# Performance work log

Measured on AMD Instinct MI355X. Metric: run time of the kernel, lower is better.

The kernel has to match this reference:

```python
import jax, jax.numpy as jnp
import numpy as np

B, S, H, KV, D = 1, 2048, 16, 4, 128
HID = H * D
CACHE = 2048
EPS = 1e-6
SCALE = 128 ** -0.5  # query_pre_attn_scalar ** -0.5
NEG = -1e9


def setup_inputs() -> dict:
    key = jax.random.key(0)
    ks = jax.random.split(key, 12)
    hidden_states = jax.random.normal(ks[0], (B, S, HID), jnp.float32)
    # rotary embeddings (Gemma3 style, base 10000, half-dim frequencies)
    pos = jnp.arange(S, dtype=jnp.float32)[:, None]
    inv_freq = 1.0 / (10000.0 ** (jnp.arange(0, D, 2, dtype=jnp.float32) / D))
    freqs = pos * inv_freq[None, :]
    emb = jnp.concatenate([freqs, freqs], axis=-1)  # [S, D]
    cos = jnp.cos(emb)[None]  # [1, S, D]
    sin = jnp.sin(emb)[None]
    # additive causal mask [B, 1, S, S]
    r = jnp.arange(S)
    attention_mask = jnp.where(r[:, None] >= r[None, :], 0.0, NEG).astype(jnp.float32)[None, None]
    lyra_key_cache = jax.random.normal(ks[1], (1, KV, CACHE, D), jnp.float32)
    lyra_value_cache = jax.random.normal(ks[2], (1, KV, CACHE, D), jnp.float32)
    w = 0.02
    Wq = jax.random.normal(ks[3], (H * D, HID), jnp.float32) * w
    Wk = jax.random.normal(ks[4], (KV * D, HID), jnp.float32) * w
    Wv = jax.random.normal(ks[5], (KV * D, HID), jnp.float32) * w
    Wo = jax.random.normal(ks[6], (HID, H * D), jnp.float32) * w
    q_norm_w = jax.random.normal(ks[7], (D,), jnp.float32) * 0.1
    k_norm_w = jax.random.normal(ks[8], (D,), jnp.float32) * 0.1
    return dict(hidden_states=hidden_states, cos=cos, sin=sin,
                attention_mask=attention_mask,
                lyra_key_cache=lyra_key_cache, lyra_value_cache=lyra_value_cache,
                Wq=Wq, Wk=Wk, Wv=Wv, Wo=Wo, q_norm_w=q_norm_w, k_norm_w=k_norm_w)


def _rmsnorm(x, w):
    xf = x.astype(jnp.float32)
    n = xf * jax.lax.rsqrt(jnp.mean(xf * xf, axis=-1, keepdims=True) + EPS)
    return (n * (1.0 + w.astype(jnp.float32))).astype(x.dtype)


def _rotate_half(x):
    h = x.shape[-1] // 2
    return jnp.concatenate([-x[..., h:], x[..., :h]], axis=-1)


def _rope(x, c, s):
    return x * c + _rotate_half(x) * s


def _attend(q, k, v, mask, n_rep):
    # q: [B,h,Sq,D]; k,v: [B,KV,Sk,D]; mask additive float broadcastable to [B,h,Sq,Sk]
    k = jnp.repeat(k, n_rep, axis=1)
    v = jnp.repeat(v, n_rep, axis=1)
    w = jnp.einsum('bhqd,bhkd->bhqk', q, k) * SCALE + mask
    w = jax.nn.softmax(w.astype(jnp.float32), axis=-1).astype(q.dtype)
    out = jnp.einsum('bhqk,bhkd->bhqd', w, v)
    return out, w


def reference(hidden_states, cos, sin, attention_mask, lyra_key_cache,
              lyra_value_cache, Wq, Wk, Wv, Wo, q_norm_w, k_norm_w):
    bsz, q_len, _ = hidden_states.shape
    q = (hidden_states @ Wq.T).reshape(bsz, q_len, H, D).transpose(0, 2, 1, 3)
    k = (hidden_states @ Wk.T).reshape(bsz, q_len, KV, D).transpose(0, 2, 1, 3)
    v = (hidden_states @ Wv.T).reshape(bsz, q_len, KV, D).transpose(0, 2, 1, 3)
    q = _rmsnorm(q, q_norm_w)
    k = _rmsnorm(k, k_norm_w)
    vanilla_q, lyra_q = q[:, :H // 2], q[:, H // 2:]
    c = cos[:, None]  # [B,1,S,D]
    s = sin[:, None]
    n_rep = (H // 2) // KV  # stream_num_key_value_groups
    # vanilla stream
    vanilla_q_rope = _rope(vanilla_q, c, s)
    k_rope = _rope(k, c, s)
    vanilla_out, vanilla_w = _attend(vanilla_q_rope, k_rope, v, attention_mask, n_rep)
    # lyra stream: prepend static KV cache; bool mask added as float (faithful to source)
    lyra_q_rope = _rope(lyra_q, c, s)
    lk = jnp.concatenate([jnp.broadcast_to(lyra_key_cache, (bsz, KV, CACHE, D)), k_rope], axis=2)
    lv = jnp.concatenate([jnp.broadcast_to(lyra_value_cache, (bsz, KV, CACHE, D)), v], axis=2)
    rows = jnp.arange(q_len)[:, None]
    cols = jnp.arange(CACHE + q_len)[None, :]
    lyra_mask = (rows < cols - CACHE).astype(jnp.float32)[None, None]  # True -> +1.0, as in torch code
    lyra_out, _ = _attend(lyra_q_rope, lk, lv, lyra_mask, n_rep)
    combined = jnp.concatenate([vanilla_out, lyra_out], axis=1)  # [B,H,S,D]
    combined = combined.transpose(0, 2, 1, 3).reshape(bsz, q_len, H * D)
    attn_output = combined @ Wo.T
    return attn_output, vanilla_w
```

## Files before the change

kernel.cpp:

```cpp
#include <hip/hip_runtime.h>
#include <math.h>

#define S_LEN 2048
#define HID 2048
#define NH 16
#define NKV 4
#define DH 128
#define CACHE_LEN 2048
#define QKV_W 3072
#define SCALE 0.08838834764831845f
#define EPS 1e-6f
#define LYRA_C 12.0f

typedef short bf16x8 __attribute__((ext_vector_type(8)));
typedef float f32x4 __attribute__((ext_vector_type(4)));

static __device__ __forceinline__ short f2bf(float x) {
  union { float f; unsigned u; } v; v.f = x;
  unsigned r = (v.u + 0x7FFF + ((v.u >> 16) & 1)) >> 16;
  return (short)r;
}

static __device__ __forceinline__ float bf2f(short h) {
  union { unsigned u; float f; } v;
  v.u = ((unsigned)(unsigned short)h) << 16;
  return v.f;
}

#define GLDS16(g, l)                                                      \
  __builtin_amdgcn_global_load_lds(                                       \
      (const __attribute__((address_space(1))) unsigned int*)(g),         \
      (__attribute__((address_space(3))) unsigned int*)(l), 16, 0, 0)

__global__ __launch_bounds__(256) void pack_bf16(
    const float* __restrict__ src, short* __restrict__ dst) {
  const int i = (blockIdx.x * 256 + threadIdx.x) * 8;
  float4 a = *(const float4*)(src + i);
  float4 b = *(const float4*)(src + i + 4);
  bf16x8 o;
  o[0] = f2bf(a.x); o[1] = f2bf(a.y); o[2] = f2bf(a.z); o[3] = f2bf(a.w);
  o[4] = f2bf(b.x); o[5] = f2bf(b.y); o[6] = f2bf(b.z); o[7] = f2bf(b.w);
  *(bf16x8*)(dst + i) = o;
}

__global__ __launch_bounds__(256) void gemm_bf16(
    const short* __restrict__ A, const short* __restrict__ B,
    float* __restrict__ C, int K, int ldc) {
  __shared__ short sA[4096];
  __shared__ short sB[4096];
  const int t = threadIdx.x;
  const int w = t >> 6;
  const int lane = t & 63;
  const int quad = lane >> 4;
  const int l16 = lane & 15;
  const int tm = blockIdx.y * 128;
  const int tn = blockIdx.x * 128;
  const int srow = lane >> 2;
  const int scol = (lane & 3) * 8;
  const int mblk = (w & 1) * 64;
  const int nblk = (w >> 1) * 64;
  f32x4 acc[4][4];
#pragma unroll
  for (int i = 0; i < 4; ++i)
#pragma unroll
    for (int j = 0; j < 4; ++j) acc[i][j] = (f32x4){0.f, 0.f, 0.f, 0.f};

  const short* Ab = A + (size_t)(tm + w * 32 + srow) * K + scol;
  const short* Bb = B + (size_t)(tn + w * 32 + srow) * K + scol;
  const size_t rstep = (size_t)16 * K;

  for (int k0 = 0; k0 < K; k0 += 32) {
    GLDS16(Ab + k0, sA + (w * 2 + 0) * 512);
    GLDS16(Ab + rstep + k0, sA + (w * 2 + 1) * 512);
    GLDS16(Bb + k0, sB + (w * 2 + 0) * 512);
    GLDS16(Bb + rstep + k0, sB + (w * 2 + 1) * 512);
    __syncthreads();
    bf16x8 af[4], bfv[4];
#pragma unroll
  for (int ms = 0; ms < 4; ++ms)
      af[ms] = *(const bf16x8*)&sA[(mblk + ms * 16 + l16) * 32 + quad * 8];
#pragma unroll
    for (int ns = 0; ns < 4; ++ns)
      bfv[ns] = *(const bf16x8*)&sB[(nblk + ns * 16 + l16) * 32 + quad * 8];
#pragma unroll
    for (int ms = 0; ms < 4; ++ms)
#pragma unroll
      for (int ns = 0; ns < 4; ++ns)
        acc[ms][ns] = __builtin_amdgcn_mfma_f32_16x16x32_bf16(
            af[ms], bfv[ns], acc[ms][ns], 0, 0, 0);
    __syncthreads();
  }
#pragma unroll
  for (int ms = 0; ms < 4; ++ms)
#pragma unroll
    for (int ns = 0; ns < 4; ++ns) {
      const int row = tm + mblk + ms * 16 + quad * 4;
      const int col = tn + nblk + ns * 16 + l16;
#pragma unroll
      for (int r = 0; r < 4; ++r)
        C[(size_t)(row + r) * ldc + col] = acc[ms][ns][r];
    }
}

__global__ __launch_bounds__(256) void rms_rope(
    float* __restrict__ qkv,
    const float* __restrict__ cosb, const float* __restrict__ sinb,
    const float* __restrict__ qw, const float* __restrict__ kw) {
  const int unit = blockIdx.x * 4 + (threadIdx.x >> 6);
  const int lane = threadIdx.x & 63;
  const int total_q = S_LEN * NH;
  float* base;
  const float* w;
  int pos;
  if (unit < total_q) {
    pos = unit >> 4;
    int head = unit & 15;
    base = qkv + (size_t)pos * QKV_W + head * DH;
    w = qw;
  } else {
    int u = unit - total_q;
    pos = u >> 2;
    int head = u & 3;
    base = qkv + (size_t)pos * QKV_W + 2048 + head * DH;
    w = kw;
  }
  float x0 = base[lane];
  float x1 = base[lane + 64];
  float ss = x0 * x0 + x1 * x1;
#pragma unroll
  for (int off = 32; off > 0; off >>= 1) ss += __shfl_xor(ss, off);
  float r = rsqrtf(ss * (1.0f / 128.0f) + EPS);
  float n0 = x0 * r * (1.0f + w[lane]);
  float n1 = x1 * r * (1.0f + w[lane + 64]);
  float c0 = cosb[(size_t)pos * DH + lane];
  float c1 = cosb[(size_t)pos * DH + lane + 64];
  float s0 = sinb[(size_t)pos * DH + lane];
  float s1 = sinb[(size_t)pos * DH + lane + 64];
  base[lane]      = n0 * c0 - n1 * s0;
  base[lane + 64] = n1 * c1 + n0 * s1;
}

__global__ __launch_bounds__(256) void pack_k(
    const float* __restrict__ qkv, const float* __restrict__ kcache,
    short* __restrict__ Kbf, short* __restrict__ Klo) {
  const int idx = blockIdx.x * 256 + threadIdx.x;
  const int e4 = idx * 4;
  const int kvh = e4 >> 19;
  const int rem = e4 & ((1 << 19) - 1);
  const int key = rem >> 7;
  const int d = rem & 127;
  const int dsw = d ^ ((key & 7) << 3);
  if (key < CACHE_LEN) {
    float4 v = *(const float4*)(kcache + (((size_t)kvh * CACHE_LEN + key) << 7) + d);
    short4 o;
    o.x = f2bf(v.x); o.y = f2bf(v.y); o.z = f2bf(v.z); o.w = f2bf(v.w);
    *(short4*)(Kbf + (size_t)(e4 - d) + dsw) = o;
  } else {
    float4 v = *(const float4*)(qkv + (size_t)(key - CACHE_LEN) * QKV_W + 2048 + kvh * DH + d);
    short4 o;
    o.x = f2bf(v.x); o.y = f2bf(v.y); o.z = f2bf(v.z); o.w = f2bf(v.w);
    *(short4*)(Kbf + (size_t)(e4 - d) + dsw) = o;
    short4 ol;
    ol.x = f2bf(v.x - bf2f(o.x));
    ol.y = f2bf(v.y - bf2f(o.y));
    ol.z = f2bf(v.z - bf2f(o.z));
    ol.w = f2bf(v.w - bf2f(o.w));
    *(short4*)(Klo + ((size_t)kvh * 2048 + (key - CACHE_LEN)) * 128 + dsw) = ol;
  }
}

__global__ __launch_bounds__(256) void pack_vt(
    const float* __restrict__ qkv, const float* __restrict__ vcache,
    short* __restrict__ Vt) {
  __shared__ float tile[64][65];
  const int key0 = blockIdx.x * 64;
  const int d0 = blockIdx.y * 64;
  const int kvh = blockIdx.z;
  const int t = threadIdx.x;
  const int c = t & 63;
  const int r0 = t >> 6;
#pragma unroll
  for (int i = 0; i < 16; ++i) {
    int r = r0 + i * 4;
    int key = key0 + r;
    float v;
    if (key < CACHE_LEN)
      v = vcache[(((size_t)kvh * CACHE_LEN + key) << 7) + d0 + c];
    else
      v = qkv[(size_t)(key - CACHE_LEN) * QKV_W + 2560 + kvh * DH + d0 + c];
    tile[r][c] = v;
  }
  __syncthreads();
#pragma unroll
  for (int i = 0; i < 16; ++i) {
    int wr = r0 + i * 4;
    int csw = c ^ (((d0 + wr) & 7) << 3);
    Vt[((size_t)kvh * DH + d0 + wr) * 4096 + key0 + csw] = f2bf(tile[c][wr]);
  }
}

static __device__ __forceinline__ void stage_kv128(
    const short* Kb, const short* Vb, short* buf, int key0, int w, int lane) {
#pragma unroll
  for (int i = 0; i < 4; ++i)
    GLDS16(Kb + ((size_t)key0 + w * 16 + i * 4) * 128 + lane * 8,
           buf + (w * 16 + i * 4) * 128);
#pragma unroll
  for (int i = 0; i < 4; ++i)
    GLDS16(Vb + (size_t)(w * 16 + i * 4 + (lane >> 4)) * 4096 + key0 +
               (lane & 15) * 8,
           buf + 16384 + (w * 16 + i * 4) * 128);
}

__global__ __launch_bounds__(512) void lyra_attn(
    const float* __restrict__ qkv,
    const short* __restrict__ Kbf,
    const short* __restrict__ Vtb,
    short* __restrict__ combined_bf) {
  __shared__ short sKV[2][32768];
  __shared__ short sP[8][2][1024];
  const int hj = blockIdx.x;
  const int qt = blockIdx.y;
  const int kvh = hj >> 1;
  const int t = threadIdx.x;
  const int w = t >> 6;
  const int lane = t & 63;
  const int quad = lane >> 4;
  const int l16 = lane & 15;
  const int wr = w >> 2;
  const int wc = w & 3;
  const int row0 = qt * 64;
  const int swx = (l16 & 7) << 4;
  const int voff = (wc >> 1) * 128 + ((((wc & 1) * 64) + quad * 16) ^ swx);

  bf16x8 qf[2][4];
#pragma unroll
  for (int g = 0; g < 2; ++g) {
    const float* qrow =
        qkv + (size_t)(row0 + wr * 32 + g * 16 + l16) * QKV_W + (8 + hj) * DH;
#pragma unroll
    for (int ks = 0; ks < 4; ++ks) {
      float4 f0 = *(const float4*)(qrow + ks * 32 + quad * 8);
      float4 f1 = *(const float4*)(qrow + ks * 32 + quad * 8 + 4);
      qf[g][ks][0] = f2bf(f0.x * SCALE); qf[g][ks][1] = f2bf(f0.y * SCALE);
      qf[g][ks][2] = f2bf(f0.z * SCALE); qf[g][ks][3] = f2bf(f0.w * SCALE);
      qf[g][ks][4] = f2bf(f1.x * SCALE); qf[g][ks][5] = f2bf(f1.y * SCALE);
      qf[g][ks][6] = f2bf(f1.z * SCALE); qf[g][ks][7] = f2bf(f1.w * SCALE);
    }
  }
  bf16x8 onesf;
#pragma unroll
  for (int i = 0; i < 8; ++i) onesf[i] = (short)0x3F80;

  f32x4 accO[2][8];
#pragma unroll
  for (int g = 0; g < 2; ++g)
#pragma unroll
    for (int i = 0; i < 8; ++i) accO[g][i] = (f32x4){0.f, 0.f, 0.f, 0.f};
  f32x4 accL[2];
  accL[0] = (f32x4){0.f, 0.f, 0.f, 0.f};
  accL[1] = (f32x4){0.f, 0.f, 0.f, 0.f};

  const short* Kb = Kbf + (size_t)kvh * 4096 * DH;
  const short* Vb = Vtb + (size_t)kvh * DH * 4096;

  stage_kv128(Kb, Vb, &sKV[0][0], 0, w, lane);

  int b = 0;
  for (int kt = 0; kt < 32; ++kt) {
    asm volatile("s_waitcnt vmcnt(0)" ::: "memory");
    __builtin_amdgcn_s_barrier();
    __builtin_amdgcn_sched_barrier(0);

    if (kt < 31)
      stage_kv128(Kb, Vb, &sKV[b ^ 1][0], (kt + 1) * 128, w, lane);

    const char* Ksc = (const char*)&sKV[b][0];
    const char* Vsc = (const char*)&sKV[b][16384];

    f32x4 accS[2][2];
#pragma unroll
    for (int g = 0; g < 2; ++g)
#pragma unroll
      for (int s = 0; s < 2; ++s)
        accS[g][s] = (f32x4){-LYRA_C, -LYRA_C, -LYRA_C, -LYRA_C};
    __builtin_amdgcn_s_setprio(1);
#pragma unroll
    for (int s = 0; s < 2; ++s) {
      const char* krow = Ksc + (wc * 32 + s * 16 + l16) * 256;
#pragma unroll
      for (int ks = 0; ks < 4; ++ks) {
        bf16x8 bk = *(const bf16x8*)(krow + ((ks * 64 + quad * 16) ^ swx));
        accS[0][s] = __builtin_amdgcn_mfma_f32_16x16x32_bf16(qf[0][ks], bk, accS[0][s], 0, 0, 0);
        accS[1][s] = __builtin_amdgcn_mfma_f32_16x16x32_bf16(qf[1][ks], bk, accS[1][s], 0, 0, 0);
      }
    }
    __builtin_amdgcn_s_setprio(0);

    const int base = kt * 128 + wc * 32;
#pragma unroll
    for (int g = 0; g < 2; ++g) {
      short* sPg = &sP[w][g][0];
#pragma unroll
      for (int s = 0; s < 2; ++s) {
        const int col = base + s * 16 + l16;
#pragma unroll
        for (int r = 0; r < 4; ++r) {
          const int row = quad * 4 + r;
          const int grow = row0 + wr * 32 + g * 16 + row;
          float z = accS[g][s][r];
          if ((col - CACHE_LEN) > grow) z += 1.0f;
          const int sl = (s * 2 + (l16 >> 3)) ^ (row & 7);
          sPg[row * 64 + sl * 8 + (l16 & 7)] = f2bf(__expf(z));
        }
      }
    }

    __builtin_amdgcn_s_setprio(1);
    bf16x8 ap0 = *(const bf16x8*)&sP[w][0][l16 * 64 + ((quad ^ (l16 & 7)) << 3)];
    bf16x8 ap1 = *(const bf16x8*)&sP[w][1][l16 * 64 + ((quad ^ (l16 & 7)) << 3)];
    accL[0] = __builtin_amdgcn_mfma_f32_16x16x32_bf16(ap0, onesf, accL[0], 0, 0, 0);
    accL[1] = __builtin_amdgcn_mfma_f32_16x16x32_bf16(ap1, onesf, accL[1], 0, 0, 0);
#pragma unroll
    for (int t8 = 0; t8 < 8; ++t8) {
      bf16x8 bv = *(const bf16x8*)(Vsc + (t8 * 16 + l16) * 256 + voff);
      accO[0][t8] = __builtin_amdgcn_mfma_f32_16x16x32_bf16(ap0, bv, accO[0][t8], 0, 0, 0);
      accO[1][t8] = __builtin_amdgcn_mfma_f32_16x16x32_bf16(ap1, bv, accO[1][t8], 0, 0, 0);
    }
    __builtin_amdgcn_s_setprio(0);

    b ^= 1;
  }

  __syncthreads();
  float* sO = (float*)&sKV[0][0];
  float* sLa = (float*)&sP[0][0][0];
  if (wc != 0) {
    float* dst = sO + (size_t)(wc - 1) * 8192;
#pragma unroll
    for (int g = 0; g < 2; ++g)
#pragma unroll
      for (int t8 = 0; t8 < 8; ++t8)
#pragma unroll
        for (int r = 0; r < 4; ++r) {
          const int rl = wr * 32 + g * 16 + quad * 4 + r;
          dst[rl * 128 + t8 * 16 + l16] = accO[g][t8][r];
        }
    if (l16 == 0) {
#pragma unroll
      for (int g = 0; g < 2; ++g)
#pragma unroll
        for (int r = 0; r < 4; ++r)
          sLa[(wc - 1) * 64 + wr * 32 + g * 16 + quad * 4 + r] = accL[g][r];
    }
  }
  __syncthreads();
  if (wc == 0) {
#pragma unroll
    for (int g = 0; g < 2; ++g) {
      float linv[4];
#pragma unroll
      for (int r = 0; r < 4; ++r) {
        const int rl = wr * 32 + g * 16 + quad * 4 + r;
        linv[r] = 1.0f / (accL[g][r] + sLa[rl] + sLa[64 + rl] + sLa[128 + rl]);
      }
#pragma unroll
      for (int t8 = 0; t8 < 8; ++t8)
#pragma unroll
        for (int r = 0; r < 4; ++r) {
          const int rl = wr * 32 + g * 16 + quad * 4 + r;
          const int c = t8 * 16 + l16;
          float o = accO[g][t8][r] + sO[rl * 128 + c] + sO[8192 + rl * 128 + c] +
                    sO[16384 + rl * 128 + c];
          combined_bf[(size_t)(row0 + rl) * HID + (8 + hj) * DH + c] =
              f2bf(o * linv[r]);
        }
    }
  }
}

__global__ __launch_bounds__(512) void vanilla_attn(
    const float* __restrict__ qkv,
    const short* __restrict__ Kbf,
    const short* __restrict__ Klo,
    const short* __restrict__ Vtb,
    float* __restrict__ wout,
    float* __restrict__ vinv,
    short* __restrict__ combined_bf) {
  __shared__ short sKV[2][32768];
  __shared__ short sP[8][2][1024];
  const int hj = blockIdx.x;
  const int qt = blockIdx.y;
  const int kvh = hj >> 1;
  const int t = threadIdx.x;
  const int w = t >> 6;
  const int lane = t & 63;
  const int quad = lane >> 4;
  const int l16 = lane & 15;
  const int wr = w >> 2;
  const int wc = w & 3;
  const int row0 = qt * 64;
  const int swx = (l16 & 7) << 4;
  const int voff = (wc >> 1) * 128 + ((((wc & 1) * 64) + quad * 16) ^ swx);
  const int nt = qt / 2 + 1;

  bf16x8 qh[2][4], ql[2][4];
#pragma unroll
  for (int g = 0; g < 2; ++g) {
    const float* qrow =
        qkv + (size_t)(row0 + wr * 32 + g * 16 + l16) * QKV_W + hj * DH;
#pragma unroll
    for (int ks = 0; ks < 4; ++ks) {
#pragma unroll
      for (int e = 0; e < 8; ++e) {
        float x = qrow[ks * 32 + quad * 8 + e] * SCALE;
        short h = f2bf(x);
        qh[g][ks][e] = h;
        ql[g][ks][e] = f2bf(x - bf2f(h));
      }
    }
  }

  f32x4 accO[2][8];
#pragma unroll
  for (int g = 0; g < 2; ++g)
#pragma unroll
    for (int i = 0; i < 8; ++i) accO[g][i] = (f32x4){0.f, 0.f, 0.f, 0.f};
  float accR[2][4] = {{0.f, 0.f, 0.f, 0.f}, {0.f, 0.f, 0.f, 0.f}};

  const short* Kh = Kbf + ((size_t)kvh * 4096 + 2048) * DH;
  const short* Kl = Klo + (size_t)kvh * 2048 * DH;
  const short* Vb = Vtb + (size_t)kvh * DH * 4096 + 2048;
  float* wrow = wout + (size_t)hj * S_LEN * S_LEN;

  stage_kv128(Kh, Vb, &sKV[0][0], 0, w, lane);

  int b = 0;
  for (int kt = 0; kt < nt; ++kt) {
    asm volatile("s_waitcnt vmcnt(0)" ::: "memory");
    __builtin_amdgcn_s_barrier();
    __builtin_amdgcn_sched_barrier(0);

    if (kt < nt - 1)
      stage_kv128(Kh, Vb, &sKV[b ^ 1][0], (kt + 1) * 128, w, lane);

    const int key0 = kt * 128;
    bf16x8 klf[2][4];
#pragma unroll
    for (int s = 0; s < 2; ++s)
#pragma unroll
      for (int ks = 0; ks < 4; ++ks)
        klf[s][ks] = *(const bf16x8*)(
            Kl + (size_t)(key0 + wc * 32 + s * 16 + l16) * 128 +
            ((ks * 32 + quad * 8) ^ ((l16 & 7) << 3)));

    const char* Khs = (const char*)&sKV[b][0];
    const char* Vsc = (const char*)&sKV[b][16384];

    f32x4 accS[2][2];
#pragma unroll
    for (int g = 0; g < 2; ++g)
#pragma unroll
      for (int s = 0; s < 2; ++s)
        accS[g][s] = (f32x4){-LYRA_C, -LYRA_C, -LYRA_C, -LYRA_C};
    __builtin_amdgcn_s_setprio(1);
#pragma unroll
    for (int s = 0; s < 2; ++s) {
      const char* krh = Khs + (wc * 32 + s * 16 + l16) * 256;
#pragma unroll
      for (int ks = 0; ks < 4; ++ks) {
        bf16x8 kh = *(const bf16x8*)(krh + ((ks * 64 + quad * 16) ^ swx));
        accS[0][s] = __builtin_amdgcn_mfma_f32_16x16x32_bf16(qh[0][ks], kh, accS[0][s], 0, 0, 0);
        accS[1][s] = __builtin_amdgcn_mfma_f32_16x16x32_bf16(qh[1][ks], kh, accS[1][s], 0, 0, 0);
        accS[0][s] = __builtin_amdgcn_mfma_f32_16x16x32_bf16(ql[0][ks], kh, accS[0][s], 0, 0, 0);
        accS[1][s] = __builtin_amdgcn_mfma_f32_16x16x32_bf16(ql[1][ks], kh, accS[1][s], 0, 0, 0);
        accS[0][s] = __builtin_amdgcn_mfma_f32_16x16x32_bf16(qh[0][ks], klf[s][ks], accS[0][s], 0, 0, 0);
        accS[1][s] = __builtin_amdgcn_mfma_f32_16x16x32_bf16(qh[1][ks], klf[s][ks], accS[1][s], 0, 0, 0);
      }
    }
    __builtin_amdgcn_s_setprio(0);

    const bool diag = (kt == nt - 1);
#pragma unroll
    for (int g = 0; g < 2; ++g) {
      short* sPg = &sP[w][g][0];
      float pr[4] = {0.f, 0.f, 0.f, 0.f};
#pragma unroll
      for (int s = 0; s < 2; ++s) {
        const int col = key0 + wc * 32 + s * 16 + l16;
#pragma unroll
        for (int r = 0; r < 4; ++r) {
          const int row = quad * 4 + r;
          const int grow = row0 + wr * 32 + g * 16 + row;
          float p = __expf(accS[g][s][r]);
          if (diag && col > grow) p = 0.f;
          pr[r] += p;
          const int sl = (s * 2 + (l16 >> 3)) ^ (row & 7);
          sPg[row * 64 + sl * 8 + (l16 & 7)] = f2bf(p);
          wrow[(size_t)grow * S_LEN + col] = p;
        }
      }
#pragma unroll
      for (int r = 0; r < 4; ++r) {
        float v = pr[r];
        v += __shfl_xor(v, 1);
        v += __shfl_xor(v, 2);
        v += __shfl_xor(v, 4);
        v += __shfl_xor(v, 8);
        accR[g][r] += v;
      }
    }

    __builtin_amdgcn_s_setprio(1);
    bf16x8 ap0 = *(const bf16x8*)&sP[w][0][l16 * 64 + ((quad ^ (l16 & 7)) << 3)];
    bf16x8 ap1 = *(const bf16x8*)&sP[w][1][l16 * 64 + ((quad ^ (l16 & 7)) << 3)];
#pragma unroll
    for (int t8 = 0; t8 < 8; ++t8) {
      bf16x8 bv = *(const bf16x8*)(Vsc + (t8 * 16 + l16) * 256 + voff);
      accO[0][t8] = __builtin_amdgcn_mfma_f32_16x16x32_bf16(ap0, bv, accO[0][t8], 0, 0, 0);
      accO[1][t8] = __builtin_amdgcn_mfma_f32_16x16x32_bf16(ap1, bv, accO[1][t8], 0, 0, 0);
    }
    __builtin_amdgcn_s_setprio(0);

    b ^= 1;
  }

  __syncthreads();
  float* sO = (float*)&sKV[0][0];
  float* sLa = (float*)&sP[0][0][0];
  if (wc != 0) {
    float* dst = sO + (size_t)(wc - 1) * 8192;
#pragma unroll
    for (int g = 0; g < 2; ++g)
#pragma unroll
      for (int t8 = 0; t8 < 8; ++t8)
#pragma unroll
        for (int r = 0; r < 4; ++r) {
          const int rl = wr * 32 + g * 16 + quad * 4 + r;
          dst[rl * 128 + t8 * 16 + l16] = accO[g][t8][r];
        }
    if (l16 == 0) {
#pragma unroll
      for (int g = 0; g < 2; ++g)
#pragma unroll
        for (int r = 0; r < 4; ++r)
          sLa[(wc - 1) * 64 + wr * 32 + g * 16 + quad * 4 + r] = accR[g][r];
    }
  }
  __syncthreads();
  if (wc == 0) {
#pragma unroll
    for (int g = 0; g < 2; ++g) {
      float linv[4];
#pragma unroll
      for (int r = 0; r < 4; ++r) {
        const int rl = wr * 32 + g * 16 + quad * 4 + r;
        linv[r] = 1.0f / (accR[g][r] + sLa[rl] + sLa[64 + rl] + sLa[128 + rl]);
      }
      if (l16 == 0) {
#pragma unroll
        for (int r = 0; r < 4; ++r)
          vinv[hj * S_LEN + row0 + wr * 32 + g * 16 + quad * 4 + r] = linv[r];
      }
#pragma unroll
      for (int t8 = 0; t8 < 8; ++t8)
#pragma unroll
        for (int r = 0; r < 4; ++r) {
          const int rl = wr * 32 + g * 16 + quad * 4 + r;
          const int c = t8 * 16 + l16;
          float o = accO[g][t8][r] + sO[rl * 128 + c] + sO[8192 + rl * 128 + c] +
                    sO[16384 + rl * 128 + c];
          combined_bf[(size_t)(row0 + rl) * HID + hj * DH + c] =
              f2bf(o * linv[r]);
        }
    }
  }
}

__global__ __launch_bounds__(256) void vnorm(
    const float* __restrict__ vinv, float* __restrict__ wout) {
  const int row = blockIdx.x;
  const int h = blockIdx.y;
  float* p = wout + (size_t)h * S_LEN * S_LEN + (size_t)row * S_LEN;
  const float inv = vinv[h * S_LEN + row];
  const int t = threadIdx.x;
#pragma unroll
  for (int i = 0; i < 2; ++i) {
    const int j = (t + i * 256) * 4;
    float4 v;
    if (j > row) {
      v = make_float4(0.f, 0.f, 0.f, 0.f);
    } else if (j + 3 <= row) {
      v = *(const float4*)(p + j);
      v.x *= inv; v.y *= inv; v.z *= inv; v.w *= inv;
    } else {
      v = *(const float4*)(p + j);
      v.x = (j + 0 <= row) ? v.x * inv : 0.f;
      v.y = (j + 1 <= row) ? v.y * inv : 0.f;
      v.z = (j + 2 <= row) ? v.z * inv : 0.f;
      v.w = (j + 3 <= row) ? v.w * inv : 0.f;
    }
    *(float4*)(p + j) = v;
  }
}

extern "C" void kernel_launch(void* const* d_in, const int* in_sizes, int n_in,
                              void* d_out, int out_size, void* d_ws, size_t ws_size,
                              hipStream_t stream) {
  (void)in_sizes; (void)n_in; (void)out_size; (void)ws_size;
  const float* hidden = (const float*)d_in[0];
  const float* cosb   = (const float*)d_in[1];
  const float* sinb   = (const float*)d_in[2];
  const float* kcache = (const float*)d_in[4];
  const float* vcache = (const float*)d_in[5];
  const float* Wq = (const float*)d_in[6];
  const float* Wk = (const float*)d_in[7];
  const float* Wv = (const float*)d_in[8];
  const float* Wo = (const float*)d_in[9];
  const float* qw = (const float*)d_in[10];
  const float* kw = (const float*)d_in[11];

  float* out  = (float*)d_out;
  float* wout = out + (size_t)4194304;

  float* qkv = (float*)d_ws;
  short* Kbf = (short*)(qkv + (size_t)2048 * QKV_W);
  short* Vtb = Kbf + (size_t)4 * 4096 * DH;
  short* combined_bf = Vtb + (size_t)4 * DH * 4096;
  short* Wo_bf = combined_bf + (size_t)2048 * HID;

  short* hidden_bf = (short*)wout;
  short* Wqkv_bf = hidden_bf + (size_t)2048 * HID;

  short* Klo  = (short*)out;
  float* vinv = (float*)(Klo + (size_t)4 * 2048 * DH);

  pack_bf16<<<dim3(2048), 256, 0, stream>>>(hidden, hidden_bf);
  pack_bf16<<<dim3(2048), 256, 0, stream>>>(Wq, Wqkv_bf);
  pack_bf16<<<dim3(512), 256, 0, stream>>>(Wk, Wqkv_bf + (size_t)2048 * 2048);
  pack_bf16<<<dim3(512), 256, 0, stream>>>(Wv, Wqkv_bf + (size_t)2560 * 2048);
  pack_bf16<<<dim3(2048), 256, 0, stream>>>(Wo, Wo_bf);

  gemm_bf16<<<dim3(24, 16), 256, 0, stream>>>(hidden_bf, Wqkv_bf, qkv, 2048, QKV_W);
  rms_rope<<<dim3(10240), 256, 0, stream>>>(qkv, cosb, sinb, qw, kw);
  pack_k<<<dim3(2048), 256, 0, stream>>>(qkv, kcache, Kbf, Klo);
  pack_vt<<<dim3(64, 2, 4), 256, 0, stream>>>(qkv, vcache, Vtb);
  lyra_attn<<<dim3(8, 32), 512, 0, stream>>>(qkv, Kbf, Vtb, combined_bf);
  vanilla_attn<<<dim3(8, 32), 512, 0, stream>>>(qkv, Kbf, Klo, Vtb, wout, vinv,
                                                combined_bf);
  vnorm<<<dim3(2048, 8), 256, 0, stream>>>(vinv, wout);
  gemm_bf16<<<dim3(16, 16), 256, 0, stream>>>(combined_bf, Wo_bf, out, 2048, HID);
}
```

Measured before the change: 495.9 us.

## Merge pack, attention and output-GEMM/vnorm launches into fewer fused kernels

Combines the five bf16 pack launches into one kernel, merges K and V packing into one launch, and runs lyra and vanilla attention as one grid with the stream chosen by block index. The output projection GEMM and the attention-weight normalisation are also merged into one launch. This cuts launch gaps and lets independent work run concurrently, but uniform-branch kernels now carry the LDS and register footprint of their largest branch. Klo and vinv move from the output buffer into workspace so the merged GEMM can write the output while vnorm reads vinv.

```diff
diff --git a/kernel.cpp b/kernel.cpp
--- a/kernel.cpp
+++ b/kernel.cpp
@@ -32,14 +32,26 @@
       (const __attribute__((address_space(1))) unsigned int*)(g),         \
       (__attribute__((address_space(3))) unsigned int*)(l), 16, 0, 0)
 
-__global__ __launch_bounds__(256) void pack_bf16(
-    const float* __restrict__ src, short* __restrict__ dst) {
-  const int i = (blockIdx.x * 256 + threadIdx.x) * 8;
+__global__ __launch_bounds__(256) void pack_all(
+    const float* __restrict__ hidden, const float* __restrict__ Wq,
+    const float* __restrict__ Wk, const float* __restrict__ Wv,
+    const float* __restrict__ Wo, short* __restrict__ hidden_bf,
+    short* __restrict__ Wqkv_bf, short* __restrict__ Wo_bf) {
+  const int b = blockIdx.x;
+  const float* src;
+  short* dst;
+  int off;
+  if (b < 2048)      { src = hidden; dst = hidden_bf; off = b; }
+  else if (b < 4096) { src = Wq; dst = Wqkv_bf; off = b - 2048; }
+  else if (b < 4608) { src = Wk; dst = Wqkv_bf + (size_t)2048 * 2048; off = b - 4096; }
+  else if (b < 5120) { src = Wv; dst = Wqkv_bf + (size_t)2560 * 2048; off = b - 4608; }
+  else               { src = Wo; dst = Wo_bf; off = b - 5120; }
+  const int i = (off * 256 + threadIdx.x) * 8;
   float4 a = *(const float4*)(src + i);
-  float4 b = *(const float4*)(src + i + 4);
+  float4 c = *(const float4*)(src + i + 4);
   bf16x8 o;
   o[0] = f2bf(a.x); o[1] = f2bf(a.y); o[2] = f2bf(a.z); o[3] = f2bf(a.w);
-  o[4] = f2bf(b.x); o[5] = f2bf(b.y); o[6] = f2bf(b.z); o[7] = f2bf(b.w);
+  o[4] = f2bf(c.x); o[5] = f2bf(c.y); o[6] = f2bf(c.z); o[7] = f2bf(c.w);
   *(bf16x8*)(dst + i) = o;
 }
 
@@ -77,7 +89,7 @@
     __syncthreads();
     bf16x8 af[4], bfv[4];
 #pragma unroll
-  for (int ms = 0; ms < 4; ++ms)
+    for (int ms = 0; ms < 4; ++ms)
       af[ms] = *(const bf16x8*)&sA[(mblk + ms * 16 + l16) * 32 + quad * 8];
 #pragma unroll
     for (int ns = 0; ns < 4; ++ns)
@@ -140,62 +152,63 @@
   base[lane + 64] = n1 * c1 + n0 * s1;
 }
 
-__global__ __launch_bounds__(256) void pack_k(
+__global__ __launch_bounds__(256) void pack_kv(
     const float* __restrict__ qkv, const float* __restrict__ kcache,
-    short* __restrict__ Kbf, short* __restrict__ Klo) {
-  const int idx = blockIdx.x * 256 + threadIdx.x;
-  const int e4 = idx * 4;
-  const int kvh = e4 >> 19;
-  const int rem = e4 & ((1 << 19) - 1);
-  const int key = rem >> 7;
-  const int d = rem & 127;
-  const int dsw = d ^ ((key & 7) << 3);
-  if (key < CACHE_LEN) {
-    float4 v = *(const float4*)(kcache + (((size_t)kvh * CACHE_LEN + key) << 7) + d);
-    short4 o;
-    o.x = f2bf(v.x); o.y = f2bf(v.y); o.z = f2bf(v.z); o.w = f2bf(v.w);
-    *(short4*)(Kbf + (size_t)(e4 - d) + dsw) = o;
+    const float* __restrict__ vcache, short* __restrict__ Kbf,
+    short* __restrict__ Klo, short* __restrict__ Vt) {
+  __shared__ float tile[64][65];
+  const int b = blockIdx.x;
+  const int t = threadIdx.x;
+  if (b < 2048) {
+    const int idx = b * 256 + t;
+    const int e4 = idx * 4;
+    const int kvh = e4 >> 19;
+    const int rem = e4 & ((1 << 19) - 1);
+    const int key = rem >> 7;
+    const int d = rem & 127;
+    const int dsw = d ^ ((key & 7) << 3);
+    if (key < CACHE_LEN) {
+      float4 v = *(const float4*)(kcache + (((size_t)kvh * CACHE_LEN + key) << 7) + d);
+      short4 o;
+      o.x = f2bf(v.x); o.y = f2bf(v.y); o.z = f2bf(v.z); o.w = f2bf(v.w);
+      *(short4*)(Kbf + (size_t)(e4 - d) + dsw) = o;
+    } else {
+      float4 v = *(const float4*)(qkv + (size_t)(key - CACHE_LEN) * QKV_W + 2048 + kvh * DH + d);
+      short4 o;
+      o.x = f2bf(v.x); o.y = f2bf(v.y); o.z = f2bf(v.z); o.w = f2bf(v.w);
+      *(short4*)(Kbf + (size_t)(e4 - d) + dsw) = o;
+      short4 ol;
+      ol.x = f2bf(v.x - bf2f(o.x));
+      ol.y = f2bf(v.y - bf2f(o.y));
+      ol.z = f2bf(v.z - bf2f(o.z));
+      ol.w = f2bf(v.w - bf2f(o.w));
+      *(short4*)(Klo + ((size_t)kvh * 2048 + (key - CACHE_LEN)) * 128 + dsw) = ol;
+    }
   } else {
-    float4 v = *(const float4*)(qkv + (size_t)(key - CACHE_LEN) * QKV_W + 2048 + kvh * DH + d);
-    short4 o;
-    o.x = f2bf(v.x); o.y = f2bf(v.y); o.z = f2bf(v.z); o.w = f2bf(v.w);
-    *(short4*)(Kbf + (size_t)(e4 - d) + dsw) = o;
-    short4 ol;
-    ol.x = f2bf(v.x - bf2f(o.x));
-    ol.y = f2bf(v.y - bf2f(o.y));
-    ol.z = f2bf(v.z - bf2f(o.z));
-    ol.w = f2bf(v.w - bf2f(o.w));
-    *(short4*)(Klo + ((size_t)kvh * 2048 + (key - CACHE_LEN)) * 128 + dsw) = ol;
-  }
-}
-
-__global__ __launch_bounds__(256) void pack_vt(
-    const float* __restrict__ qkv, const float* __restrict__ vcache,
-    short* __restrict__ Vt) {
-  __shared__ float tile[64][65];
-  const int key0 = blockIdx.x * 64;
-  const int d0 = blockIdx.y * 64;
-  const int kvh = blockIdx.z;
-  const int t = threadIdx.x;
-  const int c = t & 63;
-  const int r0 = t >> 6;
-#pragma unroll
-  for (int i = 0; i < 16; ++i) {
-    int r = r0 + i * 4;
-    int key = key0 + r;
-    float v;
-    if (key < CACHE_LEN)
-      v = vcache[(((size_t)kvh * CACHE_LEN + key) << 7) + d0 + c];
-    else
-      v = qkv[(size_t)(key - CACHE_LEN) * QKV_W + 2560 + kvh * DH + d0 + c];
-    tile[r][c] = v;
-  }
-  __syncthreads();
-#pragma unroll
-  for (int i = 0; i < 16; ++i) {
-    int wr = r0 + i * 4;
-    int csw = c ^ (((d0 + wr) & 7) << 3);
-    Vt[((size_t)kvh * DH + d0 + wr) * 4096 + key0 + csw] = f2bf(tile[c][wr]);
+    const int j = b - 2048;
+    const int key0 = (j & 63) * 64;
+    const int d0 = ((j >> 6) & 1) * 64;
+    const int kvh = j >> 7;
+    const int c = t & 63;
+    const int r0 = t >> 6;
+#pragma unroll
+    for (int i = 0; i < 16; ++i) {
+      int r = r0 + i * 4;
+      int key = key0 + r;
+      float v;
+      if (key < CACHE_LEN)
+        v = vcache[(((size_t)kvh * CACHE_LEN + key) << 7) + d0 + c];
+      else
+        v = qkv[(size_t)(key - CACHE_LEN) * QKV_W + 2560 + kvh * DH + d0 + c];
+      tile[r][c] = v;
+    }
+    __syncthreads();
+#pragma unroll
+    for (int i = 0; i < 16; ++i) {
+      int wr = r0 + i * 4;
+      int csw = c ^ (((d0 + wr) & 7) << 3);
+      Vt[((size_t)kvh * DH + d0 + wr) * 4096 + key0 + csw] = f2bf(tile[c][wr]);
+    }
   }
 }
 
@@ -212,174 +225,7 @@
            buf + 16384 + (w * 16 + i * 4) * 128);
 }
 
-__global__ __launch_bounds__(512) void lyra_attn(
-    const float* __restrict__ qkv,
-    const short* __restrict__ Kbf,
-    const short* __restrict__ Vtb,
-    short* __restrict__ combined_bf) {
-  __shared__ short sKV[2][32768];
-  __shared__ short sP[8][2][1024];
-  const int hj = blockIdx.x;
-  const int qt = blockIdx.y;
-  const int kvh = hj >> 1;
-  const int t = threadIdx.x;
-  const int w = t >> 6;
-  const int lane = t & 63;
-  const int quad = lane >> 4;
-  const int l16 = lane & 15;
-  const int wr = w >> 2;
-  const int wc = w & 3;
-  const int row0 = qt * 64;
-  const int swx = (l16 & 7) << 4;
-  const int voff = (wc >> 1) * 128 + ((((wc & 1) * 64) + quad * 16) ^ swx);
-
-  bf16x8 qf[2][4];
-#pragma unroll
-  for (int g = 0; g < 2; ++g) {
-    const float* qrow =
-        qkv + (size_t)(row0 + wr * 32 + g * 16 + l16) * QKV_W + (8 + hj) * DH;
-#pragma unroll
-    for (int ks = 0; ks < 4; ++ks) {
-      float4 f0 = *(const float4*)(qrow + ks * 32 + quad * 8);
-      float4 f1 = *(const float4*)(qrow + ks * 32 + quad * 8 + 4);
-      qf[g][ks][0] = f2bf(f0.x * SCALE); qf[g][ks][1] = f2bf(f0.y * SCALE);
-      qf[g][ks][2] = f2bf(f0.z * SCALE); qf[g][ks][3] = f2bf(f0.w * SCALE);
-      qf[g][ks][4] = f2bf(f1.x * SCALE); qf[g][ks][5] = f2bf(f1.y * SCALE);
-      qf[g][ks][6] = f2bf(f1.z * SCALE); qf[g][ks][7] = f2bf(f1.w * SCALE);
-    }
-  }
-  bf16x8 onesf;
-#pragma unroll
-  for (int i = 0; i < 8; ++i) onesf[i] = (short)0x3F80;
-
-  f32x4 accO[2][8];
-#pragma unroll
-  for (int g = 0; g < 2; ++g)
-#pragma unroll
-    for (int i = 0; i < 8; ++i) accO[g][i] = (f32x4){0.f, 0.f, 0.f, 0.f};
-  f32x4 accL[2];
-  accL[0] = (f32x4){0.f, 0.f, 0.f, 0.f};
-  accL[1] = (f32x4){0.f, 0.f, 0.f, 0.f};
-
-  const short* Kb = Kbf + (size_t)kvh * 4096 * DH;
-  const short* Vb = Vtb + (size_t)kvh * DH * 4096;
-
-  stage_kv128(Kb, Vb, &sKV[0][0], 0, w, lane);
-
-  int b = 0;
-  for (int kt = 0; kt < 32; ++kt) {
-    asm volatile("s_waitcnt vmcnt(0)" ::: "memory");
-    __builtin_amdgcn_s_barrier();
-    __builtin_amdgcn_sched_barrier(0);
-
-    if (kt < 31)
-      stage_kv128(Kb, Vb, &sKV[b ^ 1][0], (kt + 1) * 128, w, lane);
-
-    const char* Ksc = (const char*)&sKV[b][0];
-    const char* Vsc = (const char*)&sKV[b][16384];
-
-    f32x4 accS[2][2];
-#pragma unroll
-    for (int g = 0; g < 2; ++g)
-#pragma unroll
-      for (int s = 0; s < 2; ++s)
-        accS[g][s] = (f32x4){-LYRA_C, -LYRA_C, -LYRA_C, -LYRA_C};
-    __builtin_amdgcn_s_setprio(1);
-#pragma unroll
-    for (int s = 0; s < 2; ++s) {
-      const char* krow = Ksc + (wc * 32 + s * 16 + l16) * 256;
-#pragma unroll
-      for (int ks = 0; ks < 4; ++ks) {
-        bf16x8 bk = *(const bf16x8*)(krow + ((ks * 64 + quad * 16) ^ swx));
-        accS[0][s] = __builtin_amdgcn_mfma_f32_16x16x32_bf16(qf[0][ks], bk, accS[0][s], 0, 0, 0);
-        accS[1][s] = __builtin_amdgcn_mfma_f32_16x16x32_bf16(qf[1][ks], bk, accS[1][s], 0, 0, 0);
-      }
-    }
-    __builtin_amdgcn_s_setprio(0);
-
-    const int base = kt * 128 + wc * 32;
-#pragma unroll
-    for (int g = 0; g < 2; ++g) {
-      short* sPg = &sP[w][g][0];
-#pragma unroll
-      for (int s = 0; s < 2; ++s) {
-        const int col = base + s * 16 + l16;
-#pragma unroll
-        for (int r = 0; r < 4; ++r) {
-          const int row = quad * 4 + r;
-          const int grow = row0 + wr * 32 + g * 16 + row;
-          float z = accS[g][s][r];
-          if ((col - CACHE_LEN) > grow) z += 1.0f;
-          const int sl = (s * 2 + (l16 >> 3)) ^ (row & 7);
-          sPg[row * 64 + sl * 8 + (l16 & 7)] = f2bf(__expf(z));
-        }
-      }
-    }
-
-    __builtin_amdgcn_s_setprio(1);
-    bf16x8 ap0 = *(const bf16x8*)&sP[w][0][l16 * 64 + ((quad ^ (l16 & 7)) << 3)];
-    bf16x8 ap1 = *(const bf16x8*)&sP[w][1][l16 * 64 + ((quad ^ (l16 & 7)) << 3)];
-    accL[0] = __builtin_amdgcn_mfma_f32_16x16x32_bf16(ap0, onesf, accL[0], 0, 0, 0);
-    accL[1] = __builtin_amdgcn_mfma_f32_16x16x32_bf16(ap1, onesf, accL[1], 0, 0, 0);
-#pragma unroll
-    for (int t8 = 0; t8 < 8; ++t8) {
-      bf16x8 bv = *(const bf16x8*)(Vsc + (t8 * 16 + l16) * 256 + voff);
-      accO[0][t8] = __builtin_amdgcn_mfma_f32_16x16x32_bf16(ap0, bv, accO[0][t8], 0, 0, 0);
-      accO[1][t8] = __builtin_amdgcn_mfma_f32_16x16x32_bf16(ap1, bv, accO[1][t8], 0, 0, 0);
-    }
-    __builtin_amdgcn_s_setprio(0);
-
-    b ^= 1;
-  }
-
-  __syncthreads();
-  float* sO = (float*)&sKV[0][0];
-  float* sLa = (float*)&sP[0][0][0];
-  if (wc != 0) {
-    float* dst = sO + (size_t)(wc - 1) * 8192;
-#pragma unroll
-    for (int g = 0; g < 2; ++g)
-#pragma unroll
-      for (int t8 = 0; t8 < 8; ++t8)
-#pragma unroll
-        for (int r = 0; r < 4; ++r) {
-          const int rl = wr * 32 + g * 16 + quad * 4 + r;
-          dst[rl * 128 + t8 * 16 + l16] = accO[g][t8][r];
-        }
-    if (l16 == 0) {
-#pragma unroll
-      for (int g = 0; g < 2; ++g)
-#pragma unroll
-        for (int r = 0; r < 4; ++r)
-          sLa[(wc - 1) * 64 + wr * 32 + g * 16 + quad * 4 + r] = accL[g][r];
-    }
-  }
-  __syncthreads();
-  if (wc == 0) {
-#pragma unroll
-    for (int g = 0; g < 2; ++g) {
-      float linv[4];
-#pragma unroll
-      for (int r = 0; r < 4; ++r) {
-        const int rl = wr * 32 + g * 16 + quad * 4 + r;
-        linv[r] = 1.0f / (accL[g][r] + sLa[rl] + sLa[64 + rl] + sLa[128 + rl]);
-      }
-#pragma unroll
-      for (int t8 = 0; t8 < 8; ++t8)
-#pragma unroll
-        for (int r = 0; r < 4; ++r) {
-          const int rl = wr * 32 + g * 16 + quad * 4 + r;
-          const int c = t8 * 16 + l16;
-          float o = accO[g][t8][r] + sO[rl * 128 + c] + sO[8192 + rl * 128 + c] +
-                    sO[16384 + rl * 128 + c];
-          combined_bf[(size_t)(row0 + rl) * HID + (8 + hj) * DH + c] =
-              f2bf(o * linv[r]);
-        }
-    }
-  }
-}
-
-__global__ __launch_bounds__(512) void vanilla_attn(
+__global__ __launch_bounds__(512) void attn_fused(
     const float* __restrict__ qkv,
     const short* __restrict__ Kbf,
     const short* __restrict__ Klo,
@@ -389,9 +235,7 @@
     short* __restrict__ combined_bf) {
   __shared__ short sKV[2][32768];
   __shared__ short sP[8][2][1024];
-  const int hj = blockIdx.x;
-  const int qt = blockIdx.y;
-  const int kvh = hj >> 1;
+  const int bx = blockIdx.x;
   const int t = threadIdx.x;
   const int w = t >> 6;
   const int lane = t & 63;
@@ -399,208 +243,425 @@
   const int l16 = lane & 15;
   const int wr = w >> 2;
   const int wc = w & 3;
-  const int row0 = qt * 64;
   const int swx = (l16 & 7) << 4;
   const int voff = (wc >> 1) * 128 + ((((wc & 1) * 64) + quad * 16) ^ swx);
-  const int nt = qt / 2 + 1;
-
-  bf16x8 qh[2][4], ql[2][4];
-#pragma unroll
-  for (int g = 0; g < 2; ++g) {
-    const float* qrow =
-        qkv + (size_t)(row0 + wr * 32 + g * 16 + l16) * QKV_W + hj * DH;
-#pragma unroll
-    for (int ks = 0; ks < 4; ++ks) {
-#pragma unroll
-      for (int e = 0; e < 8; ++e) {
-        float x = qrow[ks * 32 + quad * 8 + e] * SCALE;
-        short h = f2bf(x);
-        qh[g][ks][e] = h;
-        ql[g][ks][e] = f2bf(x - bf2f(h));
-      }
-    }
-  }
-
-  f32x4 accO[2][8];
-#pragma unroll
-  for (int g = 0; g < 2; ++g)
-#pragma unroll
-    for (int i = 0; i < 8; ++i) accO[g][i] = (f32x4){0.f, 0.f, 0.f, 0.f};
-  float accR[2][4] = {{0.f, 0.f, 0.f, 0.f}, {0.f, 0.f, 0.f, 0.f}};
-
-  const short* Kh = Kbf + ((size_t)kvh * 4096 + 2048) * DH;
-  const short* Kl = Klo + (size_t)kvh * 2048 * DH;
-  const short* Vb = Vtb + (size_t)kvh * DH * 4096 + 2048;
-  float* wrow = wout + (size_t)hj * S_LEN * S_LEN;
-
-  stage_kv128(Kh, Vb, &sKV[0][0], 0, w, lane);
-
-  int b = 0;
-  for (int kt = 0; kt < nt; ++kt) {
-    asm volatile("s_waitcnt vmcnt(0)" ::: "memory");
-    __builtin_amdgcn_s_barrier();
-    __builtin_amdgcn_sched_barrier(0);
-
-    if (kt < nt - 1)
-      stage_kv128(Kh, Vb, &sKV[b ^ 1][0], (kt + 1) * 128, w, lane);
-
-    const int key0 = kt * 128;
-    bf16x8 klf[2][4];
-#pragma unroll
-    for (int s = 0; s < 2; ++s)
-#pragma unroll
-      for (int ks = 0; ks < 4; ++ks)
-        klf[s][ks] = *(const bf16x8*)(
-            Kl + (size_t)(key0 + wc * 32 + s * 16 + l16) * 128 +
-            ((ks * 32 + quad * 8) ^ ((l16 & 7) << 3)));
-
-    const char* Khs = (const char*)&sKV[b][0];
-    const char* Vsc = (const char*)&sKV[b][16384];
-
-    f32x4 accS[2][2];
+
+  if (bx < 8) {
+    const int hj = bx;
+    const int qt = blockIdx.y;
+    const int kvh = hj >> 1;
+    const int row0 = qt * 64;
+
+    bf16x8 qf[2][4];
+#pragma unroll
+    for (int g = 0; g < 2; ++g) {
+      const float* qrow =
+          qkv + (size_t)(row0 + wr * 32 + g * 16 + l16) * QKV_W + (8 + hj) * DH;
+#pragma unroll
+      for (int ks = 0; ks < 4; ++ks) {
+        float4 f0 = *(const float4*)(qrow + ks * 32 + quad * 8);
+        float4 f1 = *(const float4*)(qrow + ks * 32 + quad * 8 + 4);
+        qf[g][ks][0] = f2bf(f0.x * SCALE); qf[g][ks][1] = f2bf(f0.y * SCALE);
+        qf[g][ks][2] = f2bf(f0.z * SCALE); qf[g][ks][3] = f2bf(f0.w * SCALE);
+        qf[g][ks][4] = f2bf(f1.x * SCALE); qf[g][ks][5] = f2bf(f1.y * SCALE);
+        qf[g][ks][6] = f2bf(f1.z * SCALE); qf[g][ks][7] = f2bf(f1.w * SCALE);
+      }
+    }
+    bf16x8 onesf;
+#pragma unroll
+    for (int i = 0; i < 8; ++i) onesf[i] = (short)0x3F80;
+
+    f32x4 accO[2][8];
 #pragma unroll
     for (int g = 0; g < 2; ++g)
 #pragma unroll
-      for (int s = 0; s < 2; ++s)
-        accS[g][s] = (f32x4){-LYRA_C, -LYRA_C, -LYRA_C, -LYRA_C};
-    __builtin_amdgcn_s_setprio(1);
-#pragma unroll
-    for (int s = 0; s < 2; ++s) {
-      const char* krh = Khs + (wc * 32 + s * 16 + l16) * 256;
-#pragma unroll
-      for (int ks = 0; ks < 4; ++ks) {
-        bf16x8 kh = *(const bf16x8*)(krh + ((ks * 64 + quad * 16) ^ swx));
-        accS[0][s] = __builtin_amdgcn_mfma_f32_16x16x32_bf16(qh[0][ks], kh, accS[0][s], 0, 0, 0);
-        accS[1][s] = __builtin_amdgcn_mfma_f32_16x16x32_bf16(qh[1][ks], kh, accS[1][s], 0, 0, 0);
-        accS[0][s] = __builtin_amdgcn_mfma_f32_16x16x32_bf16(ql[0][ks], kh, accS[0][s], 0, 0, 0);
-        accS[1][s] = __builtin_amdgcn_mfma_f32_16x16x32_bf16(ql[1][ks], kh, accS[1][s], 0, 0, 0);
-        accS[0][s] = __builtin_amdgcn_mfma_f32_16x16x32_bf16(qh[0][ks], klf[s][ks], accS[0][s], 0, 0, 0);
-        accS[1][s] = __builtin_amdgcn_mfma_f32_16x16x32_bf16(qh[1][ks], klf[s][ks], accS[1][s], 0, 0, 0);
-      }
-    }
-    __builtin_amdgcn_s_setprio(0);
-
-    const bool diag = (kt == nt - 1);
-#pragma unroll
-    for (int g = 0; g < 2; ++g) {
-      short* sPg = &sP[w][g][0];
-      float pr[4] = {0.f, 0.f, 0.f, 0.f};
+      for (int i = 0; i < 8; ++i) accO[g][i] = (f32x4){0.f, 0.f, 0.f, 0.f};
+    f32x4 accL[2];
+    accL[0] = (f32x4){0.f, 0.f, 0.f, 0.f};
+    accL[1] = (f32x4){0.f, 0.f, 0.f, 0.f};
+
+    const short* Kb = Kbf + (size_t)kvh * 4096 * DH;
+    const short* Vb = Vtb + (size_t)kvh * DH * 4096;
+
+    stage_kv128(Kb, Vb, &sKV[0][0], 0, w, lane);
+
+    int b = 0;
+    for (int kt = 0; kt < 32; ++kt) {
+      asm volatile("s_waitcnt vmcnt(0)" ::: "memory");
+      __builtin_amdgcn_s_barrier();
+      __builtin_amdgcn_sched_barrier(0);
+
+      if (kt < 31)
+        stage_kv128(Kb, Vb, &sKV[b ^ 1][0], (kt + 1) * 128, w, lane);
+
+      const char* Ksc = (const char*)&sKV[b][0];
+      const char* Vsc = (const char*)&sKV[b][16384];
+
+      f32x4 accS[2][2];
+#pragma unroll
+      for (int g = 0; g < 2; ++g)
+#pragma unroll
+        for (int s = 0; s < 2; ++s)
+          accS[g][s] = (f32x4){-LYRA_C, -LYRA_C, -LYRA_C, -LYRA_C};
+      __builtin_amdgcn_s_setprio(1);
 #pragma unroll
       for (int s = 0; s < 2; ++s) {
-        const int col = key0 + wc * 32 + s * 16 + l16;
-#pragma unroll
-        for (int r = 0; r < 4; ++r) {
-          const int row = quad * 4 + r;
-          const int grow = row0 + wr * 32 + g * 16 + row;
-          float p = __expf(accS[g][s][r]);
-          if (diag && col > grow) p = 0.f;
-          pr[r] += p;
-          const int sl = (s * 2 + (l16 >> 3)) ^ (row & 7);
-          sPg[row * 64 + sl * 8 + (l16 & 7)] = f2bf(p);
-          wrow[(size_t)grow * S_LEN + col] = p;
-        }
-      }
-#pragma unroll
-      for (int r = 0; r < 4; ++r) {
-        float v = pr[r];
-        v += __shfl_xor(v, 1);
-        v += __shfl_xor(v, 2);
-        v += __shfl_xor(v, 4);
-        v += __shfl_xor(v, 8);
-        accR[g][r] += v;
-      }
-    }
-
-    __builtin_amdgcn_s_setprio(1);
-    bf16x8 ap0 = *(const bf16x8*)&sP[w][0][l16 * 64 + ((quad ^ (l16 & 7)) << 3)];
-    bf16x8 ap1 = *(const bf16x8*)&sP[w][1][l16 * 64 + ((quad ^ (l16 & 7)) << 3)];
-#pragma unroll
-    for (int t8 = 0; t8 < 8; ++t8) {
-      bf16x8 bv = *(const bf16x8*)(Vsc + (t8 * 16 + l16) * 256 + voff);
-      accO[0][t8] = __builtin_amdgcn_mfma_f32_16x16x32_bf16(ap0, bv, accO[0][t8], 0, 0, 0);
-      accO[1][t8] = __builtin_amdgcn_mfma_f32_16x16x32_bf16(ap1, bv, accO[1][t8], 0, 0, 0);
-    }
-    __builtin_amdgcn_s_setprio(0);
-
-    b ^= 1;
-  }
-
-  __syncthreads();
-  float* sO = (float*)&sKV[0][0];
-  float* sLa = (float*)&sP[0][0][0];
-  if (wc != 0) {
-    float* dst = sO + (size_t)(wc - 1) * 8192;
-#pragma unroll
-    for (int g = 0; g < 2; ++g)
-#pragma unroll
-      for (int t8 = 0; t8 < 8; ++t8)
+        const char* krow = Ksc + (wc * 32 + s * 16 + l16) * 256;
+#pragma unroll
+        for (int ks = 0; ks < 4; ++ks) {
+          bf16x8 bk = *(const bf16x8*)(krow + ((ks * 64 + quad * 16) ^ swx));
+          accS[0][s] = __builtin_amdgcn_mfma_f32_16x16x32_bf16(qf[0][ks], bk, accS[0][s], 0, 0, 0);
+          accS[1][s] = __builtin_amdgcn_mfma_f32_16x16x32_bf16(qf[1][ks], bk, accS[1][s], 0, 0, 0);
+        }
+      }
+      __builtin_amdgcn_s_setprio(0);
+
+      const int base = kt * 128 + wc * 32;
+#pragma unroll
+      for (int g = 0; g < 2; ++g) {
+        short* sPg = &sP[w][g][0];
+#pragma unroll
+        for (int s = 0; s < 2; ++s) {
+          const int col = base + s * 16 + l16;
+#pragma unroll
+          for (int r = 0; r < 4; ++r) {
+            const int row = quad * 4 + r;
+            const int grow = row0 + wr * 32 + g * 16 + row;
+            float z = accS[g][s][r];
+            if ((col - CACHE_LEN) > grow) z += 1.0f;
+            const int sl = (s * 2 + (l16 >> 3)) ^ (row & 7);
+            sPg[row * 64 + sl * 8 + (l16 & 7)] = f2bf(__expf(z));
+          }
+        }
+      }
+
+      __builtin_amdgcn_s_setprio(1);
+      bf16x8 ap0 = *(const bf16x8*)&sP[w][0][l16 * 64 + ((quad ^ (l16 & 7)) << 3)];
+      bf16x8 ap1 = *(const bf16x8*)&sP[w][1][l16 * 64 + ((quad ^ (l16 & 7)) << 3)];
+      accL[0] = __builtin_amdgcn_mfma_f32_16x16x32_bf16(ap0, onesf, accL[0], 0, 0, 0);
+      accL[1] = __builtin_amdgcn_mfma_f32_16x16x32_bf16(ap1, onesf, accL[1], 0, 0, 0);
+#pragma unroll
+      for (int t8 = 0; t8 < 8; ++t8) {
+        bf16x8 bv = *(const bf16x8*)(Vsc + (t8 * 16 + l16) * 256 + voff);
+        accO[0][t8] = __builtin_amdgcn_mfma_f32_16x16x32_bf16(ap0, bv, accO[0][t8], 0, 0, 0);
+        accO[1][t8] = __builtin_amdgcn_mfma_f32_16x16x32_bf16(ap1, bv, accO[1][t8], 0, 0, 0);
+      }
+      __builtin_amdgcn_s_setprio(0);
+
+      b ^= 1;
+    }
+
+    __syncthreads();
+    float* sO = (float*)&sKV[0][0];
+    float* sLa = (float*)&sP[0][0][0];
+    if (wc != 0) {
+      float* dst = sO + (size_t)(wc - 1) * 8192;
+#pragma unroll
+      for (int g = 0; g < 2; ++g)
+#pragma unroll
+        for (int t8 = 0; t8 < 8; ++t8)
+#pragma unroll
+          for (int r = 0; r < 4; ++r) {
+            const int rl = wr * 32 + g * 16 + quad * 4 + r;
+            dst[rl * 128 + t8 * 16 + l16] = accO[g][t8][r];
+          }
+      if (l16 == 0) {
+#pragma unroll
+        for (int g = 0; g < 2; ++g)
+#pragma unroll
+          for (int r = 0; r < 4; ++r)
+            sLa[(wc - 1) * 64 + wr * 32 + g * 16 + quad * 4 + r] = accL[g][r];
+      }
+    }
+    __syncthreads();
+    if (wc == 0) {
+#pragma unroll
+      for (int g = 0; g < 2; ++g) {
+        float linv[4];
 #pragma unroll
         for (int r = 0; r < 4; ++r) {
           const int rl = wr * 32 + g * 16 + quad * 4 + r;
-          dst[rl * 128 + t8 * 16 + l16] = accO[g][t8][r];
-        }
-    if (l16 == 0) {
+          linv[r] = 1.0f / (accL[g][r] + sLa[rl] + sLa[64 + rl] + sLa[128 + rl]);
+        }
+#pragma unroll
+        for (int t8 = 0; t8 < 8; ++t8)
+#pragma unroll
+          for (int r = 0; r < 4; ++r) {
+            const int rl = wr * 32 + g * 16 + quad * 4 + r;
+            const int c = t8 * 16 + l16;
+            float o = accO[g][t8][r] + sO[rl * 128 + c] + sO[8192 + rl * 128 + c] +
+                      sO[16384 + rl * 128 + c];
+            combined_bf[(size_t)(row0 + rl) * HID + (8 + hj) * DH + c] =
+                f2bf(o * linv[r]);
+          }
+      }
+    }
+  } else {
+    const int hj = bx - 8;
+    const int qt = 31 - blockIdx.y;
+    const int kvh = hj >> 1;
+    const int row0 = qt * 64;
+    const int nt = qt / 2 + 1;
+
+    bf16x8 qh[2][4], ql[2][4];
+#pragma unroll
+    for (int g = 0; g < 2; ++g) {
+      const float* qrow =
+          qkv + (size_t)(row0 + wr * 32 + g * 16 + l16) * QKV_W + hj * DH;
+#pragma unroll
+      for (int ks = 0; ks < 4; ++ks) {
+#pragma unroll
+        for (int e = 0; e < 8; ++e) {
+          float x = qrow[ks * 32 + quad * 8 + e] * SCALE;
+          short h = f2bf(x);
+          qh[g][ks][e] = h;
+          ql[g][ks][e] = f2bf(x - bf2f(h));
+        }
+      }
+    }
+
+    f32x4 accO[2][8];
+#pragma unroll
+    for (int g = 0; g < 2; ++g)
+#pragma unroll
+      for (int i = 0; i < 8; ++i) accO[g][i] = (f32x4){0.f, 0.f, 0.f, 0.f};
+    float accR[2][4] = {{0.f, 0.f, 0.f, 0.f}, {0.f, 0.f, 0.f, 0.f}};
+
+    const short* Kh = Kbf + ((size_t)kvh * 4096 + 2048) * DH;
+    const short* Kl = Klo + (size_t)kvh * 2048 * DH;
+    const short* Vb = Vtb + (size_t)kvh * DH * 4096 + 2048;
+    float* wrow = wout + (size_t)hj * S_LEN * S_LEN;
+
+    stage_kv128(Kh, Vb, &sKV[0][0], 0, w, lane);
+
+    int b = 0;
+    for (int kt = 0; kt < nt; ++kt) {
+      asm volatile("s_waitcnt vmcnt(0)" ::: "memory");
+      __builtin_amdgcn_s_barrier();
+      __builtin_amdgcn_sched_barrier(0);
+
+      if (kt < nt - 1)
+        stage_kv128(Kh, Vb, &sKV[b ^ 1][0], (kt + 1) * 128, w, lane);
+
+      const int key0 = kt * 128;
+      bf16x8 klf[2][4];
+#pragma unroll
+      for (int s = 0; s < 2; ++s)
+#pragma unroll
+        for (int ks = 0; ks < 4; ++ks)
+          klf[s][ks] = *(const bf16x8*)(
+              Kl + (size_t)(key0 + wc * 32 + s * 16 + l16) * 128 +
+              ((ks * 32 + quad * 8) ^ ((l16 & 7) << 3)));
+
+      const char* Khs = (const char*)&sKV[b][0];
+      const char* Vsc = (const char*)&sKV[b][16384];
+
+      f32x4 accS[2][2];
 #pragma unroll
       for (int g = 0; g < 2; ++g)
 #pragma unroll
-        for (int r = 0; r < 4; ++r)
-          sLa[(wc - 1) * 64 + wr * 32 + g * 16 + quad * 4 + r] = accR[g][r];
-    }
-  }
-  __syncthreads();
-  if (wc == 0) {
-#pragma unroll
-    for (int g = 0; g < 2; ++g) {
-      float linv[4];
-#pragma unroll
-      for (int r = 0; r < 4; ++r) {
-        const int rl = wr * 32 + g * 16 + quad * 4 + r;
-        linv[r] = 1.0f / (accR[g][r] + sLa[rl] + sLa[64 + rl] + sLa[128 + rl]);
-      }
+        for (int s = 0; s < 2; ++s)
+          accS[g][s] = (f32x4){-LYRA_C, -LYRA_C, -LYRA_C, -LYRA_C};
+      __builtin_amdgcn_s_setprio(1);
+#pragma unroll
+      for (int s = 0; s < 2; ++s) {
+        const char* krh = Khs + (wc * 32 + s * 16 + l16) * 256;
+#pragma unroll
+        for (int ks = 0; ks < 4; ++ks) {
+          bf16x8 kh = *(const bf16x8*)(krh + ((ks * 64 + quad * 16) ^ swx));
+          accS[0][s] = __builtin_amdgcn_mfma_f32_16x16x32_bf16(qh[0][ks], kh, accS[0][s], 0, 0, 0);
+          accS[1][s] = __builtin_amdgcn_mfma_f32_16x16x32_bf16(qh[1][ks], kh, accS[1][s], 0, 0, 0);
+          accS[0][s] = __builtin_amdgcn_mfma_f32_16x16x32_bf16(ql[0][ks], kh, accS[0][s], 0, 0, 0);
+          accS[1][s] = __builtin_amdgcn_mfma_f32_16x16x32_bf16(ql[1][ks], kh, accS[1][s], 0, 0, 0);
+          accS[0][s] = __builtin_amdgcn_mfma_f32_16x16x32_bf16(qh[0][ks], klf[s][ks], accS[0][s], 0, 0, 0);
+          accS[1][s] = __builtin_amdgcn_mfma_f32_16x16x32_bf16(qh[1][ks], klf[s][ks], accS[1][s], 0, 0, 0);
+        }
+      }
+      __builtin_amdgcn_s_setprio(0);
+
+      const bool diag = (kt == nt - 1);
+#pragma unroll
+      for (int g = 0; g < 2; ++g) {
+        short* sPg = &sP[w][g][0];
+        float pr[4] = {0.f, 0.f, 0.f, 0.f};
+#pragma unroll
+        for (int s = 0; s < 2; ++s) {
+          const int col = key0 + wc * 32 + s * 16 + l16;
+#pragma unroll
+          for (int r = 0; r < 4; ++r) {
+            const int row = quad * 4 + r;
+            const int grow = row0 + wr * 32 + g * 16 + row;
+            float p = __expf(accS[g][s][r]);
+            if (diag && col > grow) p = 0.f;
+            pr[r] += p;
+            const int sl = (s * 2 + (l16 >> 3)) ^ (row & 7);
+            sPg[row * 64 + sl * 8 + (l16 & 7)] = f2bf(p);
+            wrow[(size_t)grow * S_LEN + col] = p;
+          }
+        }
+#pragma unroll
+        for (int r = 0; r < 4; ++r) {
+          float v = pr[r];
+          v += __shfl_xor(v, 1);
+          v += __shfl_xor(v, 2);
+          v += __shfl_xor(v, 4);
+          v += __shfl_xor(v, 8);
+          accR[g][r] += v;
+        }
+      }
+
+      __builtin_amdgcn_s_setprio(1);
+      bf16x8 ap0 = *(const bf16x8*)&sP[w][0][l16 * 64 + ((quad ^ (l16 & 7)) << 3)];
+      bf16x8 ap1 = *(const bf16x8*)&sP[w][1][l16 * 64 + ((quad ^ (l16 & 7)) << 3)];
+#pragma unroll
+      for (int t8 = 0; t8 < 8; ++t8) {
+        bf16x8 bv = *(const bf16x8*)(Vsc + (t8 * 16 + l16) * 256 + voff);
+        accO[0][t8] = __builtin_amdgcn_mfma_f32_16x16x32_bf16(ap0, bv, accO[0][t8], 0, 0, 0);
+        accO[1][t8] = __builtin_amdgcn_mfma_f32_16x16x32_bf16(ap1, bv, accO[1][t8], 0, 0, 0);
+      }
+      __builtin_amdgcn_s_setprio(0);
+
+      b ^= 1;
+    }
+
+    __syncthreads();
+    float* sO = (float*)&sKV[0][0];
+    float* sLa = (float*)&sP[0][0][0];
+    if (wc != 0) {
+      float* dst = sO + (size_t)(wc - 1) * 8192;
+#pragma unroll
+      for (int g = 0; g < 2; ++g)
+#pragma unroll
+        for (int t8 = 0; t8 < 8; ++t8)
+#pragma unroll
+          for (int r = 0; r < 4; ++r) {
+            const int rl = wr * 32 + g * 16 + quad * 4 + r;
+            dst[rl * 128 + t8 * 16 + l16] = accO[g][t8][r];
+          }
       if (l16 == 0) {
 #pragma unroll
-        for (int r = 0; r < 4; ++r)
-          vinv[hj * S_LEN + row0 + wr * 32 + g * 16 + quad * 4 + r] = linv[r];
-      }
-#pragma unroll
-      for (int t8 = 0; t8 < 8; ++t8)
+        for (int g = 0; g < 2; ++g)
+#pragma unroll
+          for (int r = 0; r < 4; ++r)
+            sLa[(wc - 1) * 64 + wr * 32 + g * 16 + quad * 4 + r] = accR[g][r];
+      }
+    }
+    __syncthreads();
+    if (wc == 0) {
+#pragma unroll
+      for (int g = 0; g < 2; ++g) {
+        float linv[4];
 #pragma unroll
         for (int r = 0; r < 4; ++r) {
           const int rl = wr * 32 + g * 16 + quad * 4 + r;
-          const int c = t8 * 16 + l16;
-          float o = accO[g][t8][r] + sO[rl * 128 + c] + sO[8192 + rl * 128 + c] +
-                    sO[16384 + rl * 128 + c];
-          combined_bf[(size_t)(row0 + rl) * HID + hj * DH + c] =
-              f2bf(o * linv[r]);
-        }
+          linv[r] = 1.0f / (accR[g][r] + sLa[rl] + sLa[64 + rl] + sLa[128 + rl]);
+        }
+        if (l16 == 0) {
+#pragma unroll
+          for (int r = 0; r < 4; ++r)
+            vinv[hj * S_LEN + row0 + wr * 32 + g * 16 + quad * 4 + r] = linv[r];
+        }
+#pragma unroll
+        for (int t8 = 0; t8 < 8; ++t8)
+#pragma unroll
+          for (int r = 0; r < 4; ++r) {
+            const int rl = wr * 32 + g * 16 + quad * 4 + r;
+            const int c = t8 * 16 + l16;
+            float o = accO[g][t8][r] + sO[rl * 128 + c] + sO[8192 + rl * 128 + c] +
+                      sO[16384 + rl * 128 + c];
+            combined_bf[(size_t)(row0 + rl) * HID + hj * DH + c] =
+                f2bf(o * linv[r]);
+          }
+      }
     }
   }
 }
 
-__global__ __launch_bounds__(256) void vnorm(
-    const float* __restrict__ vinv, float* __restrict__ wout) {
-  const int row = blockIdx.x;
-  const int h = blockIdx.y;
-  float* p = wout + (size_t)h * S_LEN * S_LEN + (size_t)row * S_LEN;
-  const float inv = vinv[h * S_LEN + row];
+__global__ __launch_bounds__(256) void gemm_vnorm(
+    const short* __restrict__ A, const short* __restrict__ B,
+    float* __restrict__ C, const float* __restrict__ vinv,
+    float* __restrict__ wout) {
+  __shared__ short sA[4096];
+  __shared__ short sB[4096];
+  const int blk = blockIdx.x;
   const int t = threadIdx.x;
-#pragma unroll
-  for (int i = 0; i < 2; ++i) {
-    const int j = (t + i * 256) * 4;
-    float4 v;
-    if (j > row) {
-      v = make_float4(0.f, 0.f, 0.f, 0.f);
-    } else if (j + 3 <= row) {
-      v = *(const float4*)(p + j);
-      v.x *= inv; v.y *= inv; v.z *= inv; v.w *= inv;
-    } else {
-      v = *(const float4*)(p + j);
-      v.x = (j + 0 <= row) ? v.x * inv : 0.f;
-      v.y = (j + 1 <= row) ? v.y * inv : 0.f;
-      v.z = (j + 2 <= row) ? v.z * inv : 0.f;
-      v.w = (j + 3 <= row) ? v.w * inv : 0.f;
-    }
-    *(float4*)(p + j) = v;
+  if (blk < 256) {
+    const int K = 2048, ldc = 2048;
+    const int w = t >> 6;
+    const int lane = t & 63;
+    const int quad = lane >> 4;
+    const int l16 = lane & 15;
+    const int tm = (blk >> 4) * 128;
+    const int tn = (blk & 15) * 128;
+    const int srow = lane >> 2;
+    const int scol = (lane & 3) * 8;
+    const int mblk = (w & 1) * 64;
+    const int nblk = (w >> 1) * 64;
+    f32x4 acc[4][4];
+#pragma unroll
+    for (int i = 0; i < 4; ++i)
+#pragma unroll
+      for (int j = 0; j < 4; ++j) acc[i][j] = (f32x4){0.f, 0.f, 0.f, 0.f};
+
+    const short* Ab = A + (size_t)(tm + w * 32 + srow) * K + scol;
+    const short* Bb = B + (size_t)(tn + w * 32 + srow) * K + scol;
+    const size_t rstep = (size_t)16 * K;
+
+    for (int k0 = 0; k0 < K; k0 += 32) {
+      GLDS16(Ab + k0, sA + (w * 2 + 0) * 512);
+      GLDS16(Ab + rstep + k0, sA + (w * 2 + 1) * 512);
+      GLDS16(Bb + k0, sB + (w * 2 + 0) * 512);
+      GLDS16(Bb + rstep + k0, sB + (w * 2 + 1) * 512);
+      __syncthreads();
+      bf16x8 af[4], bfv[4];
+#pragma unroll
+      for (int ms = 0; ms < 4; ++ms)
+        af[ms] = *(const bf16x8*)&sA[(mblk + ms * 16 + l16) * 32 + quad * 8];
+#pragma unroll
+      for (int ns = 0; ns < 4; ++ns)
+        bfv[ns] = *(const bf16x8*)&sB[(nblk + ns * 16 + l16) * 32 + quad * 8];
+#pragma unroll
+      for (int ms = 0; ms < 4; ++ms)
+#pragma unroll
+        for (int ns = 0; ns < 4; ++ns)
+          acc[ms][ns] = __builtin_amdgcn_mfma_f32_16x16x32_bf16(
+              af[ms], bfv[ns], acc[ms][ns], 0, 0, 0);
+      __syncthreads();
+    }
+#pragma unroll
+    for (int ms = 0; ms < 4; ++ms)
+#pragma unroll
+      for (int ns = 0; ns < 4; ++ns) {
+        const int row = tm + mblk + ms * 16 + quad * 4;
+        const int col = tn + nblk + ns * 16 + l16;
+#pragma unroll
+        for (int r = 0; r < 4; ++r)
+          C[(size_t)(row + r) * ldc + col] = acc[ms][ns][r];
+      }
+  } else {
+    const int j0 = blk - 256;
+    const int row = j0 & 2047;
+    const int h = j0 >> 11;
+    float* p = wout + (size_t)h * S_LEN * S_LEN + (size_t)row * S_LEN;
+    const float inv = vinv[h * S_LEN + row];
+#pragma unroll
+    for (int i = 0; i < 2; ++i) {
+      const int j = (t + i * 256) * 4;
+      float4 v;
+      if (j > row) {
+        v = make_float4(0.f, 0.f, 0.f, 0.f);
+      } else if (j + 3 <= row) {
+        v = *(const float4*)(p + j);
+        v.x *= inv; v.y *= inv; v.z *= inv; v.w *= inv;
+      } else {
+        v = *(const float4*)(p + j);
+        v.x = (j + 0 <= row) ? v.x * inv : 0.f;
+        v.y = (j + 1 <= row) ? v.y * inv : 0.f;
+        v.z = (j + 2 <= row) ? v.z * inv : 0.f;
+        v.w = (j + 3 <= row) ? v.w * inv : 0.f;
+      }
+      *(float4*)(p + j) = v;
+    }
   }
 }
 
@@ -628,26 +689,18 @@
   short* Vtb = Kbf + (size_t)4 * 4096 * DH;
   short* combined_bf = Vtb + (size_t)4 * DH * 4096;
   short* Wo_bf = combined_bf + (size_t)2048 * HID;
+  short* Klo  = Wo_bf + (size_t)2048 * HID;
+  float* vinv = (float*)(Klo + (size_t)4 * 2048 * DH);
 
   short* hidden_bf = (short*)wout;
   short* Wqkv_bf = hidden_bf + (size_t)2048 * HID;
 
-  short* Klo  = (short*)out;
-  float* vinv = (float*)(Klo + (size_t)4 * 2048 * DH);
-
-  pack_bf16<<<dim3(2048), 256, 0, stream>>>(hidden, hidden_bf);
-  pack_bf16<<<dim3(2048), 256, 0, stream>>>(Wq, Wqkv_bf);
-  pack_bf16<<<dim3(512), 256, 0, stream>>>(Wk, Wqkv_bf + (size_t)2048 * 2048);
-  pack_bf16<<<dim3(512), 256, 0, stream>>>(Wv, Wqkv_bf + (size_t)2560 * 2048);
-  pack_bf16<<<dim3(2048), 256, 0, stream>>>(Wo, Wo_bf);
-
+  pack_all<<<dim3(7168), 256, 0, stream>>>(hidden, Wq, Wk, Wv, Wo,
+                                           hidden_bf, Wqkv_bf, Wo_bf);
   gemm_bf16<<<dim3(24, 16), 256, 0, stream>>>(hidden_bf, Wqkv_bf, qkv, 2048, QKV_W);
   rms_rope<<<dim3(10240), 256, 0, stream>>>(qkv, cosb, sinb, qw, kw);
-  pack_k<<<dim3(2048), 256, 0, stream>>>(qkv, kcache, Kbf, Klo);
-  pack_vt<<<dim3(64, 2, 4), 256, 0, stream>>>(qkv, vcache, Vtb);
-  lyra_attn<<<dim3(8, 32), 512, 0, stream>>>(qkv, Kbf, Vtb, combined_bf);
-  vanilla_attn<<<dim3(8, 32), 512, 0, stream>>>(qkv, Kbf, Klo, Vtb, wout, vinv,
-                                                combined_bf);
-  vnorm<<<dim3(2048, 8), 256, 0, stream>>>(vinv, wout);
-  gemm_bf16<<<dim3(16, 16), 256, 0, stream>>>(combined_bf, Wo_bf, out, 2048, HID);
-}
+  pack_kv<<<dim3(2560), 256, 0, stream>>>(qkv, kcache, vcache, Kbf, Klo, Vtb);
+  attn_fused<<<dim3(16, 32), 512, 0, stream>>>(qkv, Kbf, Klo, Vtb, wout, vinv,
+                                               combined_bf);
+  gemm_vnorm<<<dim3(16640), 256, 0, stream>>>(combined_bf, Wo_bf, out, vinv, wout);
+}
```

Result: faster. 476.2 us (-4.0%).
